# Performance work log

Hardware: AMD Instinct MI355X
Metric: run time of the kernel (lower is better)

Reference implementation:

```python
import jax, jax.numpy as jnp
from jax import lax
import numpy as np

# ---- static configuration (RPN inference path) ----
B = 8
IMG_H, IMG_W = 800, 1216
LEVEL_GRIDS = [(200, 304), (100, 152), (50, 76), (25, 38), (13, 19)]
STRIDES = [4, 8, 16, 32, 64]
SIZES = [32, 64, 128, 256, 512]
RATIOS = np.array([0.5, 1.0, 2.0])
NUM_PER_LEVEL = [h * w * 3 for (h, w) in LEVEL_GRIDS]  # [182400,45600,11400,2850,741]
A_TOTAL = sum(NUM_PER_LEVEL)                            # 242991
PRE_N = 1000   # pre_nms_top_n['testing'], applied per level
POST_N = 1000  # post_nms_top_n['testing']
NMS_THRESH = 0.7
SCORE_THRESH = 0.0
MIN_SIZE = 0.001
BBOX_XFORM_CLIP = float(np.log(1000.0 / 16.0))
LEVEL_OFFSET = 4096.0  # > max image coord, for batched_nms level separation

K_PER_LEVEL = [min(PRE_N, n) for n in NUM_PER_LEVEL]
K_TOTAL = sum(K_PER_LEVEL)  # 4741
LEVELS = jnp.concatenate([jnp.full((k,), i, dtype=jnp.int32)
                          for i, k in enumerate(K_PER_LEVEL)])


def _make_anchors():
    """torchvision-style grid anchors, one scale + 3 aspect ratios per level."""
    all_anchors = []
    for (fh, fw), stride, size in zip(LEVEL_GRIDS, STRIDES, SIZES):
        h_ratios = np.sqrt(RATIOS)
        w_ratios = 1.0 / h_ratios
        ws = w_ratios * size
        hs = h_ratios * size
        base = np.stack([-ws / 2, -hs / 2, ws / 2, hs / 2], axis=1)  # [3,4]
        sx = np.arange(fw, dtype=np.float32) * stride
        sy = np.arange(fh, dtype=np.float32) * stride
        yy, xx = np.meshgrid(sy, sx, indexing='ij')
        shifts = np.stack([xx, yy, xx, yy], axis=-1).reshape(-1, 1, 4)  # [fh*fw,1,4]
        anchors = (shifts + base[None]).reshape(-1, 4)                  # [fh*fw*3,4]
        all_anchors.append(anchors.astype(np.float32))
    return np.concatenate(all_anchors, axis=0)  # [A_TOTAL,4]


def setup_inputs() -> dict:
    key = jax.random.key(0)
    k1, k2 = jax.random.split(key)
    objectness = jax.random.normal(k1, (B, A_TOTAL), dtype=jnp.float32)
    pred_bbox_deltas = jax.random.normal(k2, (B, A_TOTAL, 4), dtype=jnp.float32) * 0.5
    anchors = jnp.asarray(_make_anchors())
    return {"objectness": objectness, "pred_bbox_deltas": pred_bbox_deltas,
            "anchors": anchors}


def _decode(deltas, anchors):
    """BoxCoder.decode with weights (1,1,1,1). deltas [B,A,4], anchors [A,4]."""
    wa = anchors[:, 2] - anchors[:, 0]
    ha = anchors[:, 3] - anchors[:, 1]
    cxa = anchors[:, 0] + 0.5 * wa
    cya = anchors[:, 1] + 0.5 * ha
    dx, dy, dw, dh = deltas[..., 0], deltas[..., 1], deltas[..., 2], deltas[..., 3]
    dw = jnp.minimum(dw, BBOX_XFORM_CLIP)
    dh = jnp.minimum(dh, BBOX_XFORM_CLIP)
    cx = dx * wa + cxa
    cy = dy * ha + cya
    w = jnp.exp(dw) * wa
    h = jnp.exp(dh) * ha
    return jnp.stack([cx - 0.5 * w, cy - 0.5 * h, cx + 0.5 * w, cy + 0.5 * h], axis=-1)


def _per_level_topk(objectness):
    """_get_top_n_idx: per-level top-k with global offsets. Returns [B,K_TOTAL] int32."""
    idxs, offset = [], 0
    for n, k in zip(NUM_PER_LEVEL, K_PER_LEVEL):
        _, ti = lax.top_k(objectness[:, offset:offset + n], k)
        idxs.append(ti + offset)
        offset += n
    return jnp.concatenate(idxs, axis=1)


def _iou(boxes):  # boxes [K,4] -> [K,K]
    area = (boxes[:, 2] - boxes[:, 0]) * (boxes[:, 3] - boxes[:, 1])
    lt = jnp.maximum(boxes[:, None, :2], boxes[None, :, :2])
    rb = jnp.minimum(boxes[:, None, 2:], boxes[None, :, 2:])
    wh = jnp.clip(rb - lt, 0.0)
    inter = wh[..., 0] * wh[..., 1]
    return inter / (area[:, None] + area[None, :] - inter)


def _nms_image(boxes, scores, levels, valid):
    """clip->filter->batched_nms->post_nms_top_n for one image (fixed shapes)."""
    K = boxes.shape[0]
    order = jnp.argsort(-jnp.where(valid, scores, -jnp.inf))
    b = boxes[order]
    s = scores[order]
    v = valid[order]
    lv = levels[order]
    # batched NMS: offset boxes by level so cross-level boxes never overlap
    bb = b + lv.astype(b.dtype)[:, None] * LEVEL_OFFSET
    iou = lax.stop_gradient(_iou(bb))  # keep decisions are non-differentiable
    idxr = jnp.arange(K)

    def body(i, keep):
        sup = (iou[i] > NMS_THRESH) & (idxr > i) & keep[i]
        return keep & ~sup

    keep = lax.fori_loop(0, K, body, v)
    sel = jnp.where(keep, s, -1.0)  # sigmoid scores are > 0
    top_s, top_i = lax.top_k(sel, POST_N)
    kept = top_s > 0.0
    out_b = jnp.where(kept[:, None], b[top_i], 0.0)
    out_s = jnp.where(kept, top_s, 0.0)
    return out_b, out_s


def reference(objectness, pred_bbox_deltas, anchors):
    # box decode for all anchors
    proposals = _decode(pred_bbox_deltas, anchors)          # [B,A,4]
    # per-level topk + gather
    idx = _per_level_topk(objectness)                       # [B,K]
    obj = jnp.take_along_axis(objectness, idx, axis=1)      # [B,K]
    props = jnp.take_along_axis(proposals, idx[..., None], axis=1)  # [B,K,4]
    scores = jax.nn.sigmoid(obj)
    lv = jnp.broadcast_to(LEVELS, idx.shape)
    # clip_boxes_to_image
    x1 = jnp.clip(props[..., 0], 0.0, IMG_W)
    y1 = jnp.clip(props[..., 1], 0.0, IMG_H)
    x2 = jnp.clip(props[..., 2], 0.0, IMG_W)
    y2 = jnp.clip(props[..., 3], 0.0, IMG_H)
    props = jnp.stack([x1, y1, x2, y2], axis=-1)
    # remove_small_boxes + score_thresh
    valid = (x2 - x1 >= MIN_SIZE) & (y2 - y1 >= MIN_SIZE) & (scores >= SCORE_THRESH)
    boxes_out, scores_out = jax.vmap(_nms_image)(props, scores, lv, valid)
    return boxes_out, scores_out  # [B,POST_N,4], [B,POST_N] (zero-padded)
```

## Files before the change

kernel.cpp:

```cpp
#include <hip/hip_runtime.h>
#include <stdint.h>

#pragma clang fp contract(off)

typedef unsigned int u32;
typedef unsigned long long u64;

#define A_TOTAL 242991
#define KTOT    4741

__constant__ int c_LN[5]   = {182400, 45600, 11400, 2850, 741};
__constant__ int c_LOFF[5] = {0, 182400, 228000, 239400, 242250};
__constant__ int c_LK[5]   = {1000, 1000, 1000, 1000, 741};

__constant__ int c_SL[33] = {0,0,0,0,0,0,0,0,0,0,0,0,0,0,0,0,0,0,0,0,0,0,0,
                             1,1,1,1,1,1, 2,2, 3, 4};
__constant__ int c_SS[33] = {0,8192,16384,24576,32768,40960,49152,57344,65536,
                             73728,81920,90112,98304,106496,114688,122880,131072,
                             139264,147456,155648,163840,172032,180224,
                             0,8192,16384,24576,32768,40960, 0,8192, 0, 0};

__constant__ int c_MW[40] = {0,1,2,3, 4,4, 5,5, 6,6, 7,7, 8,8,8, 9,9,9,
                             10,10,10, 11,11,11, 12,12,12,12, 13,13,13,13,
                             14,14,14,14, 15,15,15,15};
__constant__ int c_MR[40] = {0,0,0,0, 0,1, 0,1, 0,1, 0,1, 0,1,2, 0,1,2,
                             0,1,2, 0,1,2, 0,1,2,3, 0,1,2,3,
                             0,1,2,3, 0,1,2,3};

static const size_t OFF_KEEPW    = 0;
static const size_t OFF_HIST     = 0;
static const size_t OFF_SELCNT   = 327680;
static const size_t OFF_CANDCNT  = 327840;
static const size_t OFF_SELG     = 328320;
static const size_t OFF_CANDG    = 656000;
static const size_t OFF_BOX      = 2270144;
static const size_t OFF_SCORE    = 2876992;
static const size_t OFF_VALID    = 3028704;
static const size_t OFF_MASK     = 3180416;
static const size_t OFF_OUTK     = 8423296;

__device__ __forceinline__ u32 fmap(float f){
  u32 b = __float_as_uint(f);
  return (b & 0x80000000u) ? ~b : (b | 0x80000000u);
}
__device__ __forceinline__ float funmap(u32 m){
  return __uint_as_float((m & 0x80000000u) ? (m & 0x7FFFFFFFu) : ~m);
}

#define ZWS 82000
__global__ void __launch_bounds__(256)
k_zero(u32* __restrict__ ws0)
{
  int i = blockIdx.x * 256 + (int)threadIdx.x;
  if (i < ZWS) ws0[i] = 0u;
}

__global__ void __launch_bounds__(1024)
k_hist(const float* __restrict__ obj, u32* __restrict__ hist)
{
  int b = blockIdx.x / 33, s = blockIdx.x % 33;
  int l = c_SL[s], start = c_SS[s];
  int cnt = c_LN[l] - start; if (cnt > 8192) cnt = 8192;
  int bl = b * 5 + l;
  __shared__ u32 h[4][2048];
  for (int i = threadIdx.x; i < 8192; i += 1024) ((u32*)h)[i] = 0;
  __syncthreads();
  u32* hw = h[(threadIdx.x >> 6) & 3];
  const float* p = obj + (size_t)b * A_TOTAL + c_LOFF[l] + start;
  int head = (4 - (int)(((size_t)p >> 2) & 3)) & 3;
  if (head > cnt) head = cnt;
  if ((int)threadIdx.x < head) atomicAdd(&hw[(~fmap(p[threadIdx.x])) >> 21], 1u);
  int nvec = (cnt - head) >> 2;
  const float4* pv = (const float4*)(p + head);
  for (int i = threadIdx.x; i < nvec; i += 1024){
    float4 v = pv[i];
    atomicAdd(&hw[(~fmap(v.x)) >> 21], 1u);
    atomicAdd(&hw[(~fmap(v.y)) >> 21], 1u);
    atomicAdd(&hw[(~fmap(v.z)) >> 21], 1u);
    atomicAdd(&hw[(~fmap(v.w)) >> 21], 1u);
  }
  int tail0 = head + (nvec << 2);
  int ntail = cnt - tail0;
  if ((int)threadIdx.x < ntail) atomicAdd(&hw[(~fmap(p[tail0 + threadIdx.x])) >> 21], 1u);
  __syncthreads();
  for (int i = threadIdx.x; i < 2048; i += 1024){
    u32 v = h[0][i] + h[1][i] + h[2][i] + h[3][i];
    if (v) atomicAdd(&hist[bl * 2048 + i], v);
  }
}

#define SELCAP 2048
#define CANDCAP 1024
__global__ void __launch_bounds__(1024)
k_collect(const float* __restrict__ obj, const u32* __restrict__ hist,
          u32* __restrict__ selcnt, u32* __restrict__ candcnt,
          u64* __restrict__ selg, u64* __restrict__ candg)
{
  int b = blockIdx.x / 33, s = blockIdx.x % 33;
  int l = c_SL[s], start = c_SS[s];
  int cnt = c_LN[l] - start; if (cnt > 8192) cnt = 8192;
  int bl = b * 5 + l;
  int K = c_LK[l], n = c_LN[l];
  int tid = threadIdx.x;
  __shared__ u64 lsel[SELCAP];
  __shared__ u64 lcand[CANDCAP];
  __shared__ u32 part[1024];
  __shared__ u32 lcs, lcc, gbs, gbc, s_tval;
  if (tid == 0){ lcs = 0u; lcc = 0u; }
  if (K < n) part[tid] = hist[bl * 2048 + 2 * tid] + hist[bl * 2048 + 2 * tid + 1];
  __syncthreads();
  if (K < n && tid < 64){
    u32 gs = 0;
    #pragma unroll
    for (int q = 0; q < 16; ++q) gs += part[tid * 16 + q];
    u32 c = gs;
    for (int off = 1; off < 64; off <<= 1){
      u32 u = __shfl_up(c, off);
      if (tid >= off) c += u;
    }
    u32 cp = c - gs;
    bool crossing = (c >= (u32)K) && (cp < (u32)K);
    u64 bal = __ballot(crossing);
    int jj = __ffsll((unsigned long long)bal) - 1;
    u32 cpj = (u32)__shfl((int)cp, jj);
    u32 bv = (tid < 32) ? hist[bl * 2048 + jj * 32 + tid] : 0u;
    u32 cb = bv;
    for (int off2 = 1; off2 < 32; off2 <<= 1){
      u32 u2 = __shfl_up(cb, off2);
      if ((int)(tid & 31) >= off2) cb += u2;
    }
    bool cross2 = (tid < 32) && (cpj + cb >= (u32)K) && (cpj + cb - bv < (u32)K);
    u64 bal2 = __ballot(cross2);
    int kk = __ffsll((unsigned long long)bal2) - 1;
    if (tid == 0) s_tval = (u32)(jj * 32 + kk);
  }
  __syncthreads();
  u32 t = (K >= n) ? 2048u : s_tval;
  const float* p = obj + (size_t)b * A_TOTAL + c_LOFF[l] + start;

  auto push = [&](u32 m, int idx){
    u32 bin = m >> 21;
    u64 key = ((u64)m << 32) | (u32)idx;
    if (bin < t){
      u32 pos = atomicAdd(&lcs, 1u);
      if (pos < SELCAP) lsel[pos] = key;
      else { u32 gp = atomicAdd(&selcnt[bl], 1u); selg[(size_t)bl * 1024 + gp] = key; }
    } else if (bin == t){
      u32 pos = atomicAdd(&lcc, 1u);
      if (pos < CANDCAP) lcand[pos] = key;
      else { u32 gp = atomicAdd(&candcnt[bl], 1u); if (gp < 4096u) candg[(size_t)bl * 4096 + gp] = key; }
    }
  };

  int head = (4 - (int)(((size_t)p >> 2) & 3)) & 3;
  if (head > cnt) head = cnt;
  if (tid < head) push(~fmap(p[tid]), start + tid);
  int nvec = (cnt - head) >> 2;
  const float4* pv = (const float4*)(p + head);
  for (int i = tid; i < nvec; i += 1024){
    float4 v = pv[i];
    int e = start + head + (i << 2);
    push(~fmap(v.x), e);
    push(~fmap(v.y), e + 1);
    push(~fmap(v.z), e + 2);
    push(~fmap(v.w), e + 3);
  }
  int tail0 = head + (nvec << 2);
  int ntail = cnt - tail0;
  if (tid < ntail) push(~fmap(p[tail0 + tid]), start + tail0 + tid);
  __syncthreads();
  u32 ns = lcs;  if (ns > SELCAP) ns = SELCAP;
  u32 ncd = lcc; if (ncd > CANDCAP) ncd = CANDCAP;
  if (tid == 0){
    gbs = ns  ? atomicAdd(&selcnt[bl],  ns)  : 0u;
    gbc = ncd ? atomicAdd(&candcnt[bl], ncd) : 0u;
  }
  __syncthreads();
  u32 bs = gbs, bc = gbc;
  for (u32 i = tid; i < ns; i += 1024)
    selg[(size_t)bl * 1024 + bs + i] = lsel[i];
  for (u32 i = tid; i < ncd; i += 1024){
    u32 gp = bc + i;
    if (gp < 4096u) candg[(size_t)bl * 4096 + gp] = lcand[i];
  }
}

__global__ void __launch_bounds__(1024)
k_selectdec(const u32* __restrict__ selcnt, const u32* __restrict__ candcnt,
            const u64* __restrict__ selg, const u64* __restrict__ candg,
            const float* __restrict__ deltas, const float* __restrict__ anchors,
            float* __restrict__ boxes, float* __restrict__ scores, u32* __restrict__ valid)
{
  int bl = blockIdx.x; int b = bl / 5, l = bl % 5;
  int K = c_LK[l];
  int tid = threadIdx.x;
  __shared__ __align__(16) u64 selU[1024];
  __shared__ __align__(16) u64 candU[4098];
  __shared__ u64 keysL[1000];
  u32 ns = selcnt[bl]; if (ns > 1024u) ns = 1024u;
  u32 nc = candcnt[bl]; if (nc > 4096u) nc = 4096u;
  int R = K - (int)ns;
  selU[tid] = (tid < (int)ns) ? selg[(size_t)bl * 1024 + tid] : ~0ULL;
  for (u32 i = tid; i < nc; i += 1024) candU[i] = candg[(size_t)bl * 4096 + i];
  u32 nce = (nc + 1u) & ~1u;
  if (tid == 0 && nce > nc) candU[nc] = ~0ULL;
  __syncthreads();
  if (tid < (int)ns){
    u64 key = selU[tid];
    u32 r = 0;
    #pragma unroll 8
    for (u32 j = 0; j < 1024; j += 2){
      ulonglong2 v = *reinterpret_cast<const ulonglong2*>(&selU[j]);
      r += (v.x < key) + (v.y < key);
    }
    keysL[r] = key;
  }
  if (R > 0){
    for (u32 s = tid; s < nc; s += 1024){
      u64 key = candU[s];
      u32 r = 0;
      #pragma unroll 8
      for (u32 j = 0; j < nce; j += 2){
        ulonglong2 v = *reinterpret_cast<const ulonglong2*>(&candU[j]);
        r += (v.x < key) + (v.y < key);
      }
      if (r < (u32)R) keysL[ns + r] = key;
    }
  }
  __syncthreads();
  if (tid < K){
    u64 key = keysL[tid];
    int g = b * KTOT + l * 1000 + tid;
    u32 idx = (u32)key;
    float o = funmap(~(u32)(key >> 32));
    int ai = c_LOFF[l] + (int)idx;
    const float* a = anchors + (size_t)ai * 4;
    const float* d = deltas + ((size_t)b * A_TOTAL + ai) * 4;
    float a0 = a[0], a1 = a[1], a2 = a[2], a3 = a[3];
    float wa = __fsub_rn(a2, a0), ha = __fsub_rn(a3, a1);
    float cxa = __fadd_rn(a0, __fmul_rn(0.5f, wa));
    float cya = __fadd_rn(a1, __fmul_rn(0.5f, ha));
    float dx = d[0], dy = d[1];
    float dw = fminf(d[2], 4.135166556742356f);
    float dh = fminf(d[3], 4.135166556742356f);
    float cx = __fadd_rn(__fmul_rn(dx, wa), cxa);
    float cy = __fadd_rn(__fmul_rn(dy, ha), cya);
    float w  = __fmul_rn(expf(dw), wa);
    float h  = __fmul_rn(expf(dh), ha);
    float hw = __fmul_rn(0.5f, w), hh = __fmul_rn(0.5f, h);
    float x1 = __fsub_rn(cx, hw), y1 = __fsub_rn(cy, hh);
    float x2 = __fadd_rn(cx, hw), y2 = __fadd_rn(cy, hh);
    x1 = fminf(fmaxf(x1, 0.0f), 1216.0f);
    x2 = fminf(fmaxf(x2, 0.0f), 1216.0f);
    y1 = fminf(fmaxf(y1, 0.0f), 800.0f);
    y2 = fminf(fmaxf(y2, 0.0f), 800.0f);
    float s = __fdiv_rn(1.0f, __fadd_rn(1.0f, expf(-o)));
    int v = (__fsub_rn(x2, x1) >= 0.001f) && (__fsub_rn(y2, y1) >= 0.001f) && (s >= 0.0f);
    float* bo = boxes + (size_t)g * 4;
    bo[0] = x1; bo[1] = y1; bo[2] = x2; bo[3] = y2;
    scores[g] = s;
    valid[g] = (u32)v;
  }
}

__global__ void __launch_bounds__(256)
k_mask(const float* __restrict__ boxes, u64* __restrict__ mask)
{
  int b = blockIdx.x / 184, s = blockIdx.x % 184;
  int l, idx;
  if (s < 160){ l = s / 40; idx = s % 40; }
  else        { l = 4;      idx = s - 160; }
  int w = c_MW[idx], rb = c_MR[idx];
  int N = c_LK[l];
  int koff = l * 1000;
  float offv = (float)(l * 4096);
  __shared__ float sjx1[64], sjy1[64], sjx2[64], sjy2[64], sjar[64];
  int jbase = w * 64;
  if (threadIdx.x < 64){
    int j = jbase + (int)threadIdx.x;
    float x1, y1, x2, y2, ar;
    if (j < N){
      float4 p = ((const float4*)boxes)[(size_t)(b * KTOT + koff + j)];
      x1 = __fadd_rn(p.x, offv); y1 = __fadd_rn(p.y, offv);
      x2 = __fadd_rn(p.z, offv); y2 = __fadd_rn(p.w, offv);
      ar = __fmul_rn(__fsub_rn(x2, x1), __fsub_rn(y2, y1));
    } else {
      x1 = 3e38f; y1 = 3e38f; x2 = -3e38f; y2 = -3e38f; ar = 0.f;
    }
    sjx1[threadIdx.x] = x1; sjy1[threadIdx.x] = y1;
    sjx2[threadIdx.x] = x2; sjy2[threadIdx.x] = y2; sjar[threadIdx.x] = ar;
  }
  __syncthreads();
  int i = rb * 256 + (int)threadIdx.x;
  int rows = (w + 1) * 64; if (rows > N) rows = N;
  if (i >= rows) return;
  float4 p = ((const float4*)boxes)[(size_t)(b * KTOT + koff + i)];
  float bx1 = __fadd_rn(p.x, offv), by1 = __fadd_rn(p.y, offv);
  float bx2 = __fadd_rn(p.z, offv), by2 = __fadd_rn(p.w, offv);
  float bar = __fmul_rn(__fsub_rn(bx2, bx1), __fsub_rn(by2, by1));
  u64 bw = 0;
  #pragma unroll 16
  for (int jj = 0; jj < 64; ++jj){
    int j = jbase + jj;
    float ltx = fmaxf(bx1, sjx1[jj]), lty = fmaxf(by1, sjy1[jj]);
    float rbx = fminf(bx2, sjx2[jj]), rby = fminf(by2, sjy2[jj]);
    float wx = fmaxf(__fsub_rn(rbx, ltx), 0.0f);
    float wy = fmaxf(__fsub_rn(rby, lty), 0.0f);
    float inter = __fmul_rn(wx, wy);
    bool sup = false;
    if (inter > 0.0f && j > i){
      float den = __fsub_rn(__fadd_rn(bar, sjar[jj]), inter);
      sup = __fdiv_rn(inter, den) > 0.7f;
    }
    bw |= ((u64)sup) << jj;
  }
  mask[((size_t)(b * 5 + l) * 16 + w) * 1024 + i] = bw;
}

__global__ void __launch_bounds__(256)
k_nms(const u64* __restrict__ mask, const u32* __restrict__ valid,
      const float* __restrict__ scores, u64* __restrict__ outk,
      u64* __restrict__ keepw, float* __restrict__ outz)
{
  int bl = blockIdx.x; int b = bl / 5, l = bl % 5;
  int N = c_LK[l], koff = l * 1000;
  int WN = (N + 63) >> 6;
  int tid = threadIdx.x;
  for (int i = tid; i < 1000; i += 256) outz[bl * 1000 + i] = 0.0f;
  __shared__ u64 s_kw[16];
  __shared__ u64 s_m[7680];
  const u64* mb = mask + (size_t)bl * 16 * 1024;
  int wstage = (WN < 15) ? WN : 15;
  for (int w = 0; w < wstage; ++w){
    int rows = (w + 1) * 64;
    int base = 32 * w * (w + 1);
    for (int r = tid; r < rows; r += 256)
      s_m[base + r] = mb[(size_t)w * 1024 + r];
  }
  __syncthreads();
  if (tid < 64){
    int lane = tid;
    for (int c = 0; c < WN; ++c){
      int i = c * 64 + lane;
      int pred = (i < N) && (valid[(size_t)b * KTOT + koff + i] != 0u);
      u64 bal = __ballot(pred);
      if (lane == 0) s_kw[c] = bal;
    }
    for (int w = 0; w < WN; ++w){
      u64 kwv = s_kw[w];
      u64 supl = 0;
      if (w < 15){
        int base = 32 * w * (w + 1);
        for (int jb = 0; jb < w; ++jb){
          u64 kb = s_kw[jb];
          u64 m = s_m[base + jb * 64 + lane];
          supl |= (((kb >> lane) & 1ULL) ? m : 0ULL);
        }
      } else {
        for (int jb = 0; jb < w; ++jb){
          u64 kb = s_kw[jb];
          u64 m = mb[(size_t)w * 1024 + jb * 64 + lane];
          supl |= (((kb >> lane) & 1ULL) ? m : 0ULL);
        }
      }
      int jr = w * 64 + lane;
      u64 rowl;
      if (w < 15) rowl = s_m[32 * w * (w + 1) + jr];
      else        rowl = (jr < N) ? mb[(size_t)w * 1024 + jr] : 0ULL;
      bool inC = ((kwv >> lane) & 1ULL) != 0ULL;
      u64 rkw = rowl & kwv;
      u64 confl = inC ? rkw : 0ULL;
      u32 a0 = (u32)supl, a1 = (u32)(supl >> 32);
      u32 a2 = (u32)confl, a3 = (u32)(confl >> 32);
      for (int off = 32; off; off >>= 1){
        a0 |= __shfl_xor(a0, off);
        a1 |= __shfl_xor(a1, off);
        a2 |= __shfl_xor(a2, off);
        a3 |= __shfl_xor(a3, off);
      }
      supl = ((u64)a1 << 32) | a0;
      u64 conf = ((u64)a3 << 32) | a2;
      u64 srcb = __ballot(inC && (rkw != 0ULL));
      u64 cur = kwv & ~supl;
      u64 kept = cur;
      if (((srcb & cur) != 0ULL) && ((conf & cur) != 0ULL)){
        u32 rowl_lo = (u32)rowl, rowl_hi = (u32)(rowl >> 32);
        u64 act = cur & (srcb | conf);
        while (act){
          int ib  = __ffsll((unsigned long long)act) - 1;
          int ibs = __builtin_amdgcn_readfirstlane(ib);
          u64 bit = 1ULL << ibs;
          act &= ~bit;
          if (kept & bit){
            u32 rlo = (u32)__builtin_amdgcn_readlane((int)rowl_lo, ibs);
            u32 rhi = (u32)__builtin_amdgcn_readlane((int)rowl_hi, ibs);
            u64 r   = ((u64)rhi << 32) | rlo;
            kept &= ~r;
            act  &= ~r;
          }
        }
      }
      if (lane == 0) s_kw[w] = kept;
    }
  }
  __syncthreads();
  if (tid < 16) keepw[(size_t)bl * 16 + tid] = (tid < WN) ? s_kw[tid] : 0ULL;
  for (int i = tid; i < N; i += 256){
    u64 key = ~0ULL;
    if ((s_kw[i >> 6] >> (i & 63)) & 1ULL){
      float sc = scores[(size_t)b * KTOT + koff + i];
      key = ((u64)(~fmap(sc)) << 32) | (u32)(koff + i);
    }
    outk[(size_t)b * KTOT + koff + i] = key;
  }
}

#define CMPN 1024
__global__ void __launch_bounds__(256)
k_rank(const u64* __restrict__ outk, const u64* __restrict__ keepw,
       const float* __restrict__ boxes, float* __restrict__ out)
{
  int b = blockIdx.x / 19, chunk = blockIdx.x % 19;
  int tid = threadIdx.x;
  __shared__ u64 cmp[5 * CMPN];
  __shared__ u64 kw[80];
  for (int i = tid; i < 5 * CMPN; i += 256) cmp[i] = ~0ULL;
  if (tid < 80) kw[tid] = keepw[(size_t)b * 80 + tid];
  __syncthreads();
  for (int i = tid; i < KTOT; i += 256){
    u64 key = outk[(size_t)b * KTOT + i];
    if (key != ~0ULL){
      int l = i / 1000; if (l > 4) l = 4;
      int li = i - l * 1000;
      int wi = li >> 6, bit = li & 63;
      const u64* kwl = &kw[l * 16];
      int r = __popcll(kwl[wi] & ((1ULL << bit) - 1ULL));
      for (int w = 0; w < wi; ++w) r += __popcll(kwl[w]);
      cmp[l * CMPN + r] = key;
    }
  }
  __syncthreads();
  int i = chunk * 256 + tid;
  if (i >= KTOT) return;
  u64 key = outk[(size_t)b * KTOT + i];
  if (key == ~0ULL) return;
  int l = i / 1000; if (l > 4) l = 4;
  int li = i - l * 1000;
  int wi = li >> 6, bit = li & 63;
  const u64* kwl = &kw[l * 16];
  int rank = __popcll(kwl[wi] & ((1ULL << bit) - 1ULL));
  for (int w = 0; w < wi; ++w) rank += __popcll(kwl[w]);
  #pragma unroll
  for (int lo = 0; lo < 5; ++lo){
    if (lo == l) continue;
    int pos = 0;
    #pragma unroll
    for (int s = 512; s > 0; s >>= 1)
      if (cmp[lo * CMPN + pos + s - 1] < key) pos += s;
    rank += pos;
  }
  if (rank < 1000){
    float4 bx = ((const float4*)boxes)[(size_t)(b * KTOT + i)];
    ((float4*)out)[(size_t)(b * 1000 + rank)] = bx;
    out[32000 + b * 1000 + rank] = funmap(~(u32)(key >> 32));
  }
}

extern "C" void kernel_launch(void* const* d_in, const int* in_sizes, int n_in,
                              void* d_out, int out_size, void* d_ws, size_t ws_size,
                              hipStream_t stream)
{
  (void)in_sizes; (void)n_in; (void)out_size; (void)ws_size;
  const float* obj     = (const float*)d_in[0];
  const float* deltas  = (const float*)d_in[1];
  const float* anchors = (const float*)d_in[2];
  float* out = (float*)d_out;
  char* ws = (char*)d_ws;

  u32* hist    = (u32*)(ws + OFF_HIST);
  u64* keepw   = (u64*)(ws + OFF_KEEPW);
  u32* selcnt  = (u32*)(ws + OFF_SELCNT);
  u32* candcnt = (u32*)(ws + OFF_CANDCNT);
  u64* selg    = (u64*)(ws + OFF_SELG);
  u64* candg   = (u64*)(ws + OFF_CANDG);
  float* boxes = (float*)(ws + OFF_BOX);
  float* score = (float*)(ws + OFF_SCORE);
  u32* valid   = (u32*)(ws + OFF_VALID);
  u64* mask    = (u64*)(ws + OFF_MASK);
  u64* outk    = (u64*)(ws + OFF_OUTK);

  hipLaunchKernelGGL(k_zero,      dim3((ZWS + 255) / 256), dim3(256), 0, stream, (u32*)ws);
  hipLaunchKernelGGL(k_hist,      dim3(264),  dim3(1024), 0, stream, obj, hist);
  hipLaunchKernelGGL(k_collect,   dim3(264),  dim3(1024), 0, stream, obj, hist, selcnt, candcnt, selg, candg);
  hipLaunchKernelGGL(k_selectdec, dim3(40),   dim3(1024), 0, stream, selcnt, candcnt, selg, candg,
                     deltas, anchors, boxes, score, valid);
  hipLaunchKernelGGL(k_mask,      dim3(1472), dim3(256),  0, stream, boxes, mask);
  hipLaunchKernelGGL(k_nms,       dim3(40),   dim3(256),  0, stream, mask, valid, score, outk, keepw, out);
  hipLaunchKernelGGL(k_rank,      dim3(152),  dim3(256),  0, stream, outk, keepw, boxes, out);
}
```

Before: 125.0 us.

## Fuse select/decode, IoU mask and NMS into one per-level block kernel

Merges k_selectdec, k_mask and k_nms into a single kernel with 40 blocks of 1024 threads. Decoded boxes, areas, scores and valid flags stay in shared memory, and the suppression mask is built in shared memory instead of global memory. This removes two launches and the global round trips for boxes, scores, valid flags and the mask. In exchange, the IoU mask work that previously ran on 1472 blocks now runs on only 40 blocks, which cuts parallelism, and the large shared-memory footprint limits occupancy.

```diff
diff --git a/kernel.cpp b/kernel.cpp
--- a/kernel.cpp
+++ b/kernel.cpp
@@ -5,6 +5,7 @@
 
 typedef unsigned int u32;
 typedef unsigned long long u64;
+typedef unsigned char u8;
 
 #define A_TOTAL 242991
 #define KTOT    4741
@@ -19,13 +20,6 @@
                              73728,81920,90112,98304,106496,114688,122880,131072,
                              139264,147456,155648,163840,172032,180224,
                              0,8192,16384,24576,32768,40960, 0,8192, 0, 0};
-
-__constant__ int c_MW[40] = {0,1,2,3, 4,4, 5,5, 6,6, 7,7, 8,8,8, 9,9,9,
-                             10,10,10, 11,11,11, 12,12,12,12, 13,13,13,13,
-                             14,14,14,14, 15,15,15,15};
-__constant__ int c_MR[40] = {0,0,0,0, 0,1, 0,1, 0,1, 0,1, 0,1,2, 0,1,2,
-                             0,1,2, 0,1,2, 0,1,2,3, 0,1,2,3,
-                             0,1,2,3, 0,1,2,3};
 
 static const size_t OFF_KEEPW    = 0;
 static const size_t OFF_HIST     = 0;
@@ -34,9 +28,6 @@
 static const size_t OFF_SELG     = 328320;
 static const size_t OFF_CANDG    = 656000;
 static const size_t OFF_BOX      = 2270144;
-static const size_t OFF_SCORE    = 2876992;
-static const size_t OFF_VALID    = 3028704;
-static const size_t OFF_MASK     = 3180416;
 static const size_t OFF_OUTK     = 8423296;
 
 __device__ __forceinline__ u32 fmap(float f){
@@ -186,17 +177,27 @@
 }
 
 __global__ void __launch_bounds__(1024)
-k_selectdec(const u32* __restrict__ selcnt, const u32* __restrict__ candcnt,
-            const u64* __restrict__ selg, const u64* __restrict__ candg,
-            const float* __restrict__ deltas, const float* __restrict__ anchors,
-            float* __restrict__ boxes, float* __restrict__ scores, u32* __restrict__ valid)
+k_sdmn(const u32* __restrict__ selcnt, const u32* __restrict__ candcnt,
+       const u64* __restrict__ selg, const u64* __restrict__ candg,
+       const float* __restrict__ deltas, const float* __restrict__ anchors,
+       float* __restrict__ boxes, u64* __restrict__ outk,
+       u64* __restrict__ keepw, float* __restrict__ outz)
 {
   int bl = blockIdx.x; int b = bl / 5, l = bl % 5;
   int K = c_LK[l];
+  int N = K;
+  int koff = l * 1000;
+  int WN = (N + 63) >> 6;
   int tid = threadIdx.x;
-  __shared__ __align__(16) u64 selU[1024];
-  __shared__ __align__(16) u64 candU[4098];
+  __shared__ __align__(16) u64 buf[8704];
   __shared__ u64 keysL[1000];
+  __shared__ float bx1L[1024], by1L[1024], bx2L[1024], by2L[1024], arL[1024], scoresL[1024];
+  __shared__ u8  validB[1024];
+  __shared__ u64 s_kw[16];
+  u64* selU  = buf;
+  u64* candU = buf + 1024;
+  for (int i = tid; i < 1000; i += 256) if (tid < 256) outz[bl * 1000 + i] = 0.0f;
+  for (int i = tid; i < 1000; i += 1024) outz[bl * 1000 + i] = 0.0f;
   u32 ns = selcnt[bl]; if (ns > 1024u) ns = 1024u;
   u32 nc = candcnt[bl]; if (nc > 4096u) nc = 4096u;
   int R = K - (int)ns;
@@ -205,15 +206,15 @@
   u32 nce = (nc + 1u) & ~1u;
   if (tid == 0 && nce > nc) candU[nc] = ~0ULL;
   __syncthreads();
+  u64 mykey = (tid < (int)ns) ? selU[tid] : ~0ULL;
   if (tid < (int)ns){
-    u64 key = selU[tid];
     u32 r = 0;
     #pragma unroll 8
     for (u32 j = 0; j < 1024; j += 2){
       ulonglong2 v = *reinterpret_cast<const ulonglong2*>(&selU[j]);
-      r += (v.x < key) + (v.y < key);
-    }
-    keysL[r] = key;
+      r += (v.x < mykey) + (v.y < mykey);
+    }
+    keysL[r] = mykey;
   }
   if (R > 0){
     for (u32 s = tid; s < nc; s += 1024){
@@ -228,9 +229,10 @@
     }
   }
   __syncthreads();
+  float offv = (float)(l * 4096);
   if (tid < K){
     u64 key = keysL[tid];
-    int g = b * KTOT + l * 1000 + tid;
+    int g = b * KTOT + koff + tid;
     u32 idx = (u32)key;
     float o = funmap(~(u32)(key >> 32));
     int ai = c_LOFF[l] + (int)idx;
@@ -254,119 +256,67 @@
     x2 = fminf(fmaxf(x2, 0.0f), 1216.0f);
     y1 = fminf(fmaxf(y1, 0.0f), 800.0f);
     y2 = fminf(fmaxf(y2, 0.0f), 800.0f);
-    float s = __fdiv_rn(1.0f, __fadd_rn(1.0f, expf(-o)));
-    int v = (__fsub_rn(x2, x1) >= 0.001f) && (__fsub_rn(y2, y1) >= 0.001f) && (s >= 0.0f);
+    float sc = __fdiv_rn(1.0f, __fadd_rn(1.0f, expf(-o)));
+    int v = (__fsub_rn(x2, x1) >= 0.001f) && (__fsub_rn(y2, y1) >= 0.001f) && (sc >= 0.0f);
     float* bo = boxes + (size_t)g * 4;
     bo[0] = x1; bo[1] = y1; bo[2] = x2; bo[3] = y2;
-    scores[g] = s;
-    valid[g] = (u32)v;
-  }
-}
-
-__global__ void __launch_bounds__(256)
-k_mask(const float* __restrict__ boxes, u64* __restrict__ mask)
-{
-  int b = blockIdx.x / 184, s = blockIdx.x % 184;
-  int l, idx;
-  if (s < 160){ l = s / 40; idx = s % 40; }
-  else        { l = 4;      idx = s - 160; }
-  int w = c_MW[idx], rb = c_MR[idx];
-  int N = c_LK[l];
-  int koff = l * 1000;
-  float offv = (float)(l * 4096);
-  __shared__ float sjx1[64], sjy1[64], sjx2[64], sjy2[64], sjar[64];
-  int jbase = w * 64;
-  if (threadIdx.x < 64){
-    int j = jbase + (int)threadIdx.x;
-    float x1, y1, x2, y2, ar;
-    if (j < N){
-      float4 p = ((const float4*)boxes)[(size_t)(b * KTOT + koff + j)];
-      x1 = __fadd_rn(p.x, offv); y1 = __fadd_rn(p.y, offv);
-      x2 = __fadd_rn(p.z, offv); y2 = __fadd_rn(p.w, offv);
-      ar = __fmul_rn(__fsub_rn(x2, x1), __fsub_rn(y2, y1));
-    } else {
-      x1 = 3e38f; y1 = 3e38f; x2 = -3e38f; y2 = -3e38f; ar = 0.f;
-    }
-    sjx1[threadIdx.x] = x1; sjy1[threadIdx.x] = y1;
-    sjx2[threadIdx.x] = x2; sjy2[threadIdx.x] = y2; sjar[threadIdx.x] = ar;
-  }
-  __syncthreads();
-  int i = rb * 256 + (int)threadIdx.x;
-  int rows = (w + 1) * 64; if (rows > N) rows = N;
-  if (i >= rows) return;
-  float4 p = ((const float4*)boxes)[(size_t)(b * KTOT + koff + i)];
-  float bx1 = __fadd_rn(p.x, offv), by1 = __fadd_rn(p.y, offv);
-  float bx2 = __fadd_rn(p.z, offv), by2 = __fadd_rn(p.w, offv);
-  float bar = __fmul_rn(__fsub_rn(bx2, bx1), __fsub_rn(by2, by1));
-  u64 bw = 0;
-  #pragma unroll 16
-  for (int jj = 0; jj < 64; ++jj){
-    int j = jbase + jj;
-    float ltx = fmaxf(bx1, sjx1[jj]), lty = fmaxf(by1, sjy1[jj]);
-    float rbx = fminf(bx2, sjx2[jj]), rby = fminf(by2, sjy2[jj]);
-    float wx = fmaxf(__fsub_rn(rbx, ltx), 0.0f);
-    float wy = fmaxf(__fsub_rn(rby, lty), 0.0f);
-    float inter = __fmul_rn(wx, wy);
-    bool sup = false;
-    if (inter > 0.0f && j > i){
-      float den = __fsub_rn(__fadd_rn(bar, sjar[jj]), inter);
-      sup = __fdiv_rn(inter, den) > 0.7f;
-    }
-    bw |= ((u64)sup) << jj;
-  }
-  mask[((size_t)(b * 5 + l) * 16 + w) * 1024 + i] = bw;
-}
-
-__global__ void __launch_bounds__(256)
-k_nms(const u64* __restrict__ mask, const u32* __restrict__ valid,
-      const float* __restrict__ scores, u64* __restrict__ outk,
-      u64* __restrict__ keepw, float* __restrict__ outz)
-{
-  int bl = blockIdx.x; int b = bl / 5, l = bl % 5;
-  int N = c_LK[l], koff = l * 1000;
-  int WN = (N + 63) >> 6;
-  int tid = threadIdx.x;
-  for (int i = tid; i < 1000; i += 256) outz[bl * 1000 + i] = 0.0f;
-  __shared__ u64 s_kw[16];
-  __shared__ u64 s_m[7680];
-  const u64* mb = mask + (size_t)bl * 16 * 1024;
-  int wstage = (WN < 15) ? WN : 15;
-  for (int w = 0; w < wstage; ++w){
-    int rows = (w + 1) * 64;
+    float ox1 = __fadd_rn(x1, offv), oy1 = __fadd_rn(y1, offv);
+    float ox2 = __fadd_rn(x2, offv), oy2 = __fadd_rn(y2, offv);
+    bx1L[tid] = ox1; by1L[tid] = oy1; bx2L[tid] = ox2; by2L[tid] = oy2;
+    arL[tid] = __fmul_rn(__fsub_rn(ox2, ox1), __fsub_rn(oy2, oy1));
+    scoresL[tid] = sc;
+    validB[tid] = (u8)v;
+  } else {
+    bx1L[tid] = 3e38f; by1L[tid] = 3e38f; bx2L[tid] = -3e38f; by2L[tid] = -3e38f;
+    arL[tid] = 0.f; scoresL[tid] = 0.f; validB[tid] = 0;
+  }
+  __syncthreads();
+  u64* s_m = buf;
+  for (int w = 0; w < WN; ++w){
+    int rowsw = (w + 1) * 64; if (rowsw > N) rowsw = N;
     int base = 32 * w * (w + 1);
-    for (int r = tid; r < rows; r += 256)
-      s_m[base + r] = mb[(size_t)w * 1024 + r];
+    int jbase = w * 64;
+    for (int i = tid; i < rowsw; i += 1024){
+      float bx1 = bx1L[i], by1 = by1L[i], bx2 = bx2L[i], by2 = by2L[i], bar = arL[i];
+      u64 bw = 0;
+      #pragma unroll 16
+      for (int jj = 0; jj < 64; ++jj){
+        int j = jbase + jj;
+        float ltx = fmaxf(bx1, bx1L[j]), lty = fmaxf(by1, by1L[j]);
+        float rbx = fminf(bx2, bx2L[j]), rby = fminf(by2, by2L[j]);
+        float wx = fmaxf(__fsub_rn(rbx, ltx), 0.0f);
+        float wy = fmaxf(__fsub_rn(rby, lty), 0.0f);
+        float inter = __fmul_rn(wx, wy);
+        bool sup = false;
+        if (inter > 0.0f && j > i){
+          float den = __fsub_rn(__fadd_rn(bar, arL[j]), inter);
+          sup = __fdiv_rn(inter, den) > 0.7f;
+        }
+        bw |= ((u64)sup) << jj;
+      }
+      s_m[base + i] = bw;
+    }
   }
   __syncthreads();
   if (tid < 64){
     int lane = tid;
     for (int c = 0; c < WN; ++c){
       int i = c * 64 + lane;
-      int pred = (i < N) && (valid[(size_t)b * KTOT + koff + i] != 0u);
+      int pred = (i < N) && (validB[i] != 0);
       u64 bal = __ballot(pred);
       if (lane == 0) s_kw[c] = bal;
     }
     for (int w = 0; w < WN; ++w){
       u64 kwv = s_kw[w];
+      int base = 32 * w * (w + 1);
       u64 supl = 0;
-      if (w < 15){
-        int base = 32 * w * (w + 1);
-        for (int jb = 0; jb < w; ++jb){
-          u64 kb = s_kw[jb];
-          u64 m = s_m[base + jb * 64 + lane];
-          supl |= (((kb >> lane) & 1ULL) ? m : 0ULL);
-        }
-      } else {
-        for (int jb = 0; jb < w; ++jb){
-          u64 kb = s_kw[jb];
-          u64 m = mb[(size_t)w * 1024 + jb * 64 + lane];
-          supl |= (((kb >> lane) & 1ULL) ? m : 0ULL);
-        }
+      for (int jb = 0; jb < w; ++jb){
+        u64 kb = s_kw[jb];
+        u64 m = s_m[base + jb * 64 + lane];
+        supl |= (((kb >> lane) & 1ULL) ? m : 0ULL);
       }
       int jr = w * 64 + lane;
-      u64 rowl;
-      if (w < 15) rowl = s_m[32 * w * (w + 1) + jr];
-      else        rowl = (jr < N) ? mb[(size_t)w * 1024 + jr] : 0ULL;
+      u64 rowl = (jr < N) ? s_m[base + jr] : 0ULL;
       bool inC = ((kwv >> lane) & 1ULL) != 0ULL;
       u64 rkw = rowl & kwv;
       u64 confl = inC ? rkw : 0ULL;
@@ -405,10 +355,10 @@
   }
   __syncthreads();
   if (tid < 16) keepw[(size_t)bl * 16 + tid] = (tid < WN) ? s_kw[tid] : 0ULL;
-  for (int i = tid; i < N; i += 256){
+  for (int i = tid; i < N; i += 1024){
     u64 key = ~0ULL;
     if ((s_kw[i >> 6] >> (i & 63)) & 1ULL){
-      float sc = scores[(size_t)b * KTOT + koff + i];
+      float sc = scoresL[i];
       key = ((u64)(~fmap(sc)) << 32) | (u32)(koff + i);
     }
     outk[(size_t)b * KTOT + koff + i] = key;
@@ -484,17 +434,12 @@
   u64* selg    = (u64*)(ws + OFF_SELG);
   u64* candg   = (u64*)(ws + OFF_CANDG);
   float* boxes = (float*)(ws + OFF_BOX);
-  float* score = (float*)(ws + OFF_SCORE);
-  u32* valid   = (u32*)(ws + OFF_VALID);
-  u64* mask    = (u64*)(ws + OFF_MASK);
   u64* outk    = (u64*)(ws + OFF_OUTK);
 
-  hipLaunchKernelGGL(k_zero,      dim3((ZWS + 255) / 256), dim3(256), 0, stream, (u32*)ws);
-  hipLaunchKernelGGL(k_hist,      dim3(264),  dim3(1024), 0, stream, obj, hist);
-  hipLaunchKernelGGL(k_collect,   dim3(264),  dim3(1024), 0, stream, obj, hist, selcnt, candcnt, selg, candg);
-  hipLaunchKernelGGL(k_selectdec, dim3(40),   dim3(1024), 0, stream, selcnt, candcnt, selg, candg,
-                     deltas, anchors, boxes, score, valid);
-  hipLaunchKernelGGL(k_mask,      dim3(1472), dim3(256),  0, stream, boxes, mask);
-  hipLaunchKernelGGL(k_nms,       dim3(40),   dim3(256),  0, stream, mask, valid, score, outk, keepw, out);
-  hipLaunchKernelGGL(k_rank,      dim3(152),  dim3(256),  0, stream, outk, keepw, boxes, out);
-}
+  hipLaunchKernelGGL(k_zero,    dim3((ZWS + 255) / 256), dim3(256), 0, stream, (u32*)ws);
+  hipLaunchKernelGGL(k_hist,    dim3(264), dim3(1024), 0, stream, obj, hist);
+  hipLaunchKernelGGL(k_collect, dim3(264), dim3(1024), 0, stream, obj, hist, selcnt, candcnt, selg, candg);
+  hipLaunchKernelGGL(k_sdmn,    dim3(40),  dim3(1024), 0, stream, selcnt, candcnt, selg, candg,
+                     deltas, anchors, boxes, outk, keepw, out);
+  hipLaunchKernelGGL(k_rank,    dim3(152), dim3(256),  0, stream, outk, keepw, boxes, out);
+}
```

Result: slower. 232.3 us (+85.9%).
